# Kernel optimization log

Hardware: AMD Instinct MI355X
Metric: run time of the kernel (lower is better)

## Reference

```python
import jax, jax.numpy as jnp
import numpy as np

N = 100000   # nodes
E = 1600000  # edges (before self-loops)
G = 128      # graphs in batch
IN = 128     # in_channels
H = 64       # GCN hidden dim
OUT = 7      # out_channels
N_STACK = 9  # 64->64 GCN layers after the first


def setup_inputs() -> dict:
    key = jax.random.key(0)
    ks = jax.random.split(key, 10)
    s = 0.1
    x = jax.random.normal(ks[0], (N, IN), dtype=jnp.float32)
    edge_index = jax.random.randint(ks[1], (2, E), 0, N, dtype=jnp.int32)
    batch = jnp.sort(jax.random.randint(ks[2], (N,), 0, G, dtype=jnp.int32))
    W0 = jax.random.normal(ks[3], (IN, H), dtype=jnp.float32) * s
    b0 = jnp.zeros((H,), dtype=jnp.float32)
    Ws = jax.random.normal(ks[4], (N_STACK, H, H), dtype=jnp.float32) * s
    bs = jnp.zeros((N_STACK, H), dtype=jnp.float32)
    Wlin = jax.random.normal(ks[5], (H, OUT), dtype=jnp.float32) * s
    blin = jnp.zeros((OUT,), dtype=jnp.float32)
    return {"x": x, "edge_index": edge_index, "batch": batch,
            "W0": W0, "b0": b0, "Ws": Ws, "bs": bs,
            "Wlin": Wlin, "blin": blin}


def reference(x, edge_index, batch, W0, b0, Ws, bs, Wlin, blin):
    # GCNConv with add_self_loops=True, normalize=True (PyG defaults):
    # out = D^{-1/2} (A + I) D^{-1/2} (X W) + b
    loop = jnp.arange(N, dtype=edge_index.dtype)
    src = jnp.concatenate([edge_index[0], loop])   # [E+N]
    dst = jnp.concatenate([edge_index[1], loop])   # [E+N]
    ones = jnp.ones_like(dst, dtype=x.dtype)
    deg = jax.ops.segment_sum(ones, dst, num_segments=N)       # in-degree incl. self-loop
    dinv = jnp.where(deg > 0, jax.lax.rsqrt(deg), 0.0)
    norm = dinv[src] * dinv[dst]                                # [E+N]

    def gcn(h, W, b):
        m = h @ W                                               # [N,H] linear first
        agg = jax.ops.segment_sum(norm[:, None] * m[src], dst, num_segments=N)
        return agg + b

    h = jax.nn.relu(gcn(x, W0, b0))
    # nn.Dropout / EvalDropout are identity in the deterministic reference

    def step(h, wb):
        W, b = wb
        return jax.nn.relu(gcn(h, W, b)), None

    h, _ = jax.lax.scan(step, h, (Ws, bs))                      # 9 stacked GCN layers

    # global_mean_pool over graph ids
    counts = jax.ops.segment_sum(jnp.ones((N,), dtype=h.dtype), batch, num_segments=G)
    pooled = jax.ops.segment_sum(h, batch, num_segments=G) / jnp.clip(counts, 1.0)[:, None]
    return pooled @ Wlin + blin                                 # [G, OUT]
```

## Files before the change

kernel.cpp:

```cpp
#include <hip/hip_runtime.h>
#include <hip/hip_fp16.h>

#define NNODES 100000
#define NEDGES 1600000
#define NGRAPH 128
#define CIN 128
#define CH 64
#define COUT 7
#define NSTACK 9

#define NB 391
#define CHUNK 2048
#define NC 782

typedef __attribute__((ext_vector_type(8))) short bf16x8;
typedef __attribute__((ext_vector_type(4))) float f32x4;

__device__ __forceinline__ unsigned short f2bf(float f) {
    unsigned u = __float_as_uint(f);
    return (unsigned short)((u + 0x7FFFu + ((u >> 16) & 1u)) >> 16);
}

__global__ __launch_bounds__(256) void hist_gemm_kernel(const int* __restrict__ dst,
                                                        int* __restrict__ hist, int E,
                                                        const float* __restrict__ h,
                                                        const float* __restrict__ W,
                                                        __half* __restrict__ m, int N,
                                                        int histBlocks) {
    __shared__ alignas(16) char smem[32768 + 2048];
    if (blockIdx.x < (unsigned)histBlocks) {
        int* lh = (int*)smem;
        for (int i = threadIdx.x; i < NB; i += 256) lh[i] = 0;
        __syncthreads();
        int e0 = blockIdx.x * CHUNK;
        int e1 = min(e0 + CHUNK, E);
        for (int e = e0 + threadIdx.x; e < e1; e += 256)
            atomicAdd(&lh[dst[e] >> 8], 1);
        __syncthreads();
        for (int i = threadIdx.x; i < NB; i += 256) hist[i * NC + (int)blockIdx.x] = lh[i];
        return;
    }
    int gb = blockIdx.x - histBlocks;
    unsigned short* wf_hi = (unsigned short*)smem;
    unsigned short* wf_lo = wf_hi + 16 * 64 * 8;
    int t = threadIdx.x;

    {
        int c = t >> 4;
        int kstep = c >> 2, ncol = c & 3;
        int l0 = (t & 15) * 4;
        for (int dl = 0; dl < 4; ++dl) {
            int l = l0 + dl;
            int kbase = kstep * 32 + (l >> 4) * 8;
            int n = ncol * 16 + (l & 15);
            for (int i = 0; i < 8; ++i) {
                float wv = W[(size_t)(kbase + i) * 64 + n];
                unsigned short hb = f2bf(wv);
                float hf = __uint_as_float(((unsigned)hb) << 16);
                wf_hi[((size_t)c * 64 + l) * 8 + i] = hb;
                wf_lo[((size_t)c * 64 + l) * 8 + i] = f2bf(wv - hf);
            }
        }
    }
    __syncthreads();

    int wave = t >> 6, lane = t & 63;
    long row0 = (long)gb * 64 + wave * 16;
    if (row0 >= N) return;

    long arow = row0 + (lane & 15);
    const float4* xr = (const float4*)(h + (size_t)arow * 128);
    int kg = lane >> 4;

    f32x4 zero = {0.0f, 0.0f, 0.0f, 0.0f};
    f32x4 acc[4];
    acc[0] = zero; acc[1] = zero; acc[2] = zero; acc[3] = zero;

#pragma unroll
    for (int s = 0; s < 4; ++s) {
        float4 p = xr[s * 8 + kg * 2];
        float4 q = xr[s * 8 + kg * 2 + 1];
        float xv[8] = {p.x, p.y, p.z, p.w, q.x, q.y, q.z, q.w};
        bf16x8 a_hi, a_lo;
#pragma unroll
        for (int i = 0; i < 8; ++i) {
            unsigned short hb = f2bf(xv[i]);
            a_hi[i] = (short)hb;
            a_lo[i] = (short)f2bf(xv[i] - __uint_as_float(((unsigned)hb) << 16));
        }
#pragma unroll
        for (int nc = 0; nc < 4; ++nc) {
            int c = s * 4 + nc;
            bf16x8 b_hi = *(const bf16x8*)(wf_hi + ((size_t)c * 64 + lane) * 8);
            bf16x8 b_lo = *(const bf16x8*)(wf_lo + ((size_t)c * 64 + lane) * 8);
            acc[nc] = __builtin_amdgcn_mfma_f32_16x16x32_bf16(a_hi, b_hi, acc[nc], 0, 0, 0);
            acc[nc] = __builtin_amdgcn_mfma_f32_16x16x32_bf16(a_hi, b_lo, acc[nc], 0, 0, 0);
            acc[nc] = __builtin_amdgcn_mfma_f32_16x16x32_bf16(a_lo, b_hi, acc[nc], 0, 0, 0);
        }
    }

    int drow = (lane >> 4) * 4;
    int dcol = lane & 15;
#pragma unroll
    for (int nc = 0; nc < 4; ++nc)
#pragma unroll
        for (int r = 0; r < 4; ++r)
            m[(size_t)(row0 + drow + r) * 64 + nc * 16 + dcol] = __float2half(acc[nc][r]);
}

__global__ __launch_bounds__(256) void scan_chunks_kernel(int* __restrict__ hist,
                                                          int* __restrict__ btot) {
    int b = blockIdx.x;
    int t = threadIdx.x;
    int* row = hist + b * NC;
    int v[4];
    int base = 4 * t;
#pragma unroll
    for (int u = 0; u < 4; ++u) v[u] = (base + u < NC) ? row[base + u] : 0;
    int tsum = v[0] + v[1] + v[2] + v[3];
    __shared__ int s[256];
    s[t] = tsum;
    __syncthreads();
    for (int d = 1; d < 256; d <<= 1) {
        int x = (t >= d) ? s[t - d] : 0;
        __syncthreads();
        s[t] += x;
        __syncthreads();
    }
    int run = s[t] - tsum;
    if (t == 255) btot[b] = s[255];
#pragma unroll
    for (int u = 0; u < 4; ++u) {
        if (base + u < NC) row[base + u] = run;
        run += v[u];
    }
}

__global__ void scan_buckets_kernel(const int* __restrict__ tot, int* __restrict__ out) {
    __shared__ int s[512];
    int t = threadIdx.x;
    int v = (t < NB) ? tot[t] : 0;
    s[t] = v;
    __syncthreads();
    for (int d = 1; d < 512; d <<= 1) {
        int x = (t >= d) ? s[t - d] : 0;
        __syncthreads();
        s[t] += x;
        __syncthreads();
    }
    if (t < NB) out[t] = s[t] - v;
    if (t == NB - 1) out[NB] = s[t];
}

__global__ __launch_bounds__(256) void scatter_kernel(const int* __restrict__ src,
                                                      const int* __restrict__ dst,
                                                      const int* __restrict__ hist,
                                                      const int* __restrict__ bbase,
                                                      int* __restrict__ src_b,
                                                      int* __restrict__ dst_b, int E) {
    __shared__ int offs[NB];
    for (int b = threadIdx.x; b < NB; b += 256)
        offs[b] = hist[b * NC + (int)blockIdx.x] + bbase[b];
    __syncthreads();
    int e0 = blockIdx.x * CHUNK;
    int e1 = min(e0 + CHUNK, E);
    for (int e = e0 + threadIdx.x; e < e1; e += 256) {
        int d = dst[e], s = src[e];
        int pos = atomicAdd(&offs[d >> 8], 1);
        src_b[pos] = s;
        dst_b[pos] = d;
    }
}

__global__ __launch_bounds__(256) void bucket_prep_kernel(const int* __restrict__ dst_b,
                                                          const int* __restrict__ bbase,
                                                          const int* __restrict__ btot,
                                                          int* __restrict__ rowptr,
                                                          int* __restrict__ pbt,
                                                          float* __restrict__ dinv,
                                                          const int* __restrict__ batch,
                                                          int* __restrict__ gcnt, int N) {
    if ((int)blockIdx.x == NB) {
        int g = threadIdx.x;
        if (g >= NGRAPH) return;
        auto lb = [&](int v) {
            int lo = 0, hi = N;
            while (lo < hi) {
                int mid = (lo + hi) >> 1;
                if (batch[mid] < v) lo = mid + 1; else hi = mid;
            }
            return lo;
        };
        gcnt[g] = lb(g + 1) - lb(g);
        return;
    }
    __shared__ int c256[256];
    __shared__ int s[256];
    int t = threadIdx.x;
    c256[t] = 0;
    __syncthreads();
    int lo = bbase[blockIdx.x], n = btot[blockIdx.x];
    for (int e = lo + t; e < lo + n; e += 256) atomicAdd(&c256[dst_b[e] & 255], 1);
    __syncthreads();
    int cnt = c256[t];
    int pcnt = (cnt + 7) & ~7;
    s[t] = pcnt;
    __syncthreads();
    for (int d = 1; d < 256; d <<= 1) {
        int x = (t >= d) ? s[t - d] : 0;
        __syncthreads();
        s[t] += x;
        __syncthreads();
    }
    int node = blockIdx.x * 256 + t;
    if (node < N) {
        rowptr[node] = s[t] - pcnt;
        dinv[node] = 1.0f / sqrtf((float)(cnt + 1));
    }
    if (t == 255) pbt[blockIdx.x] = s[255];
}

__global__ void rowptr_fix_kernel(int* __restrict__ rowptr, const int* __restrict__ pbbase,
                                  int N) {
    int i = blockIdx.x * 256 + threadIdx.x;
    if (i < N) rowptr[i] += pbbase[i >> 8];
    if (i == 0) rowptr[N] = pbbase[NB];
}

__global__ __launch_bounds__(256) void bucket_fill_kernel(const int* __restrict__ src_b,
                                                          const int* __restrict__ dst_b,
                                                          const int* __restrict__ bbase,
                                                          const int* __restrict__ btot,
                                                          const int* __restrict__ rowptr,
                                                          int* __restrict__ col, int N) {
    __shared__ int f256[256];
    __shared__ int rp[256];
    int t = threadIdx.x;
    f256[t] = 0;
    int node = blockIdx.x * 256 + t;
    rp[t] = (node < N) ? rowptr[node] : 0;
    __syncthreads();
    int lo = bbase[blockIdx.x], n = btot[blockIdx.x];
    for (int e = lo + t; e < lo + n; e += 256) {
        int d = dst_b[e], sv = src_b[e];
        int li = d & 255;
        int slot = atomicAdd(&f256[li], 1);
        col[rp[li] + slot] = sv;
    }
    __syncthreads();
    if (node < N) {
        int c = f256[t];
        int pc = (c + 7) & ~7;
        int base = rp[t];
        for (int p = c; p < pc; ++p) col[base + p] = N;
    }
}

__global__ __launch_bounds__(256) void scale_m_kernel(__half* __restrict__ m,
                                                      __half* __restrict__ other,
                                                      const float* __restrict__ dinv, int N) {
    if (blockIdx.x == 0 && threadIdx.x < 64) {
        m[(size_t)N * 64 + threadIdx.x] = __float2half(0.0f);
        other[(size_t)N * 64 + threadIdx.x] = __float2half(0.0f);
    }
    int tot = N * 32;
    __half2* m2 = (__half2*)m;
    for (int idx = blockIdx.x * 256 + threadIdx.x; idx < tot; idx += gridDim.x * 256) {
        float d = dinv[idx >> 5];
        float2 f = __half22float2(m2[idx]);
        f.x *= d;
        f.y *= d;
        m2[idx] = __float22half2_rn(f);
    }
}

__device__ __forceinline__ void pair_gather(const __half* __restrict__ h,
                                            const int* __restrict__ col,
                                            int r0, int mid, int r1, int lane,
                                            float& aA, float& aB) {
    int n = r1 - r0;
    int e = 0;
    for (; e + 16 <= n; e += 16) {
        int base = r0 + e;
        int c[16];
        float v[16];
#pragma unroll
        for (int u = 0; u < 16; ++u) c[u] = col[base + u];
#pragma unroll
        for (int u = 0; u < 16; ++u) v[u] = __half2float(h[(size_t)c[u] * 64 + lane]);
        float s0 = ((v[0] + v[1]) + (v[2] + v[3])) + ((v[4] + v[5]) + (v[6] + v[7]));
        float s1 = ((v[8] + v[9]) + (v[10] + v[11])) + ((v[12] + v[13]) + (v[14] + v[15]));
        bool b0 = (base < mid);
        bool b1 = (base + 8 < mid);
        aA += b0 ? s0 : 0.0f;
        aB += b0 ? 0.0f : s0;
        aA += b1 ? s1 : 0.0f;
        aB += b1 ? 0.0f : s1;
    }
    if (e + 8 <= n) {
        int base = r0 + e;
        int c[8];
        float v[8];
#pragma unroll
        for (int u = 0; u < 8; ++u) c[u] = col[base + u];
#pragma unroll
        for (int u = 0; u < 8; ++u) v[u] = __half2float(h[(size_t)c[u] * 64 + lane]);
        float s0 = ((v[0] + v[1]) + (v[2] + v[3])) + ((v[4] + v[5]) + (v[6] + v[7]));
        bool b0 = (base < mid);
        aA += b0 ? s0 : 0.0f;
        aB += b0 ? 0.0f : s0;
    }
}

__global__ __launch_bounds__(256) void agg0_kernel(const __half* __restrict__ m,
                                                   const int* __restrict__ rowptr,
                                                   const int* __restrict__ col,
                                                   const float* __restrict__ dinv,
                                                   const float* __restrict__ bias,
                                                   __half* __restrict__ hout, int N) {
    int wid = __builtin_amdgcn_readfirstlane((blockIdx.x * 256 + threadIdx.x) >> 6);
    int lane = threadIdx.x & 63;
    int nodeA = wid * 2;
    int nodeB = nodeA + 1;
    if (nodeA >= N) return;
    int r0 = rowptr[nodeA];
    int mid = rowptr[nodeB];
    int r1 = rowptr[nodeB + 1];
    float diA = dinv[nodeA], diB = dinv[nodeB];
    float aA = __half2float(m[(size_t)nodeA * 64 + lane]);
    float aB = __half2float(m[(size_t)nodeB * 64 + lane]);
    pair_gather(m, col, r0, mid, r1, lane, aA, aB);
    float bv = bias[lane];
    float hA = fmaxf(diA * aA + bv, 0.0f);
    float hB = fmaxf(diB * aB + bv, 0.0f);
    hout[(size_t)nodeA * 64 + lane] = __float2half(diA * hA);
    hout[(size_t)nodeB * 64 + lane] = __float2half(diB * hB);
}

__global__ __launch_bounds__(256) void fused_kernel(const __half* __restrict__ h,
                                                    const int* __restrict__ rowptr,
                                                    const int* __restrict__ col,
                                                    const float* __restrict__ dinv,
                                                    const float* __restrict__ W,
                                                    const float* __restrict__ bias,
                                                    __half* __restrict__ hout, int N,
                                                    int scaleOut) {
    __shared__ float Ws[64 * 64];
    {
        const float4* W4 = (const float4*)W;
        float4* Ws4 = (float4*)Ws;
        for (int i = threadIdx.x; i < 64 * 16; i += 256) Ws4[i] = W4[i];
    }

    int wid = __builtin_amdgcn_readfirstlane((blockIdx.x * 256 + threadIdx.x) >> 6);
    int lane = threadIdx.x & 63;
    int nodeA = wid * 2;
    int nodeB = nodeA + 1;
    bool act = (nodeA < N);
    float gA = 0.0f, gB = 0.0f;
    float diA = 0.0f, diB = 0.0f;

    if (act) {
        int r0 = rowptr[nodeA];
        int mid = rowptr[nodeB];
        int r1 = rowptr[nodeB + 1];
        diA = dinv[nodeA];
        diB = dinv[nodeB];
        float aA = __half2float(h[(size_t)nodeA * 64 + lane]);
        float aB = __half2float(h[(size_t)nodeB * 64 + lane]);
        pair_gather(h, col, r0, mid, r1, lane, aA, aB);
        gA = diA * aA;
        gB = diB * aB;
    }

    __syncthreads();

    if (act) {
        float bv = bias[lane];
        float accA = bv, accB = bv;
#pragma unroll
        for (int k = 0; k < 64; ++k) {
            float wv = Ws[k * 64 + lane];
            unsigned ga = __builtin_amdgcn_readlane(__float_as_uint(gA), k);
            unsigned gb = __builtin_amdgcn_readlane(__float_as_uint(gB), k);
            accA += __uint_as_float(ga) * wv;
            accB += __uint_as_float(gb) * wv;
        }
        accA = fmaxf(accA, 0.0f);
        accB = fmaxf(accB, 0.0f);
        if (scaleOut) { accA *= diA; accB *= diB; }
        hout[(size_t)nodeA * 64 + lane] = __float2half(accA);
        hout[(size_t)nodeB * 64 + lane] = __float2half(accB);
    }
}

__global__ __launch_bounds__(256) void pool_kernel(const __half* __restrict__ h,
                                                   const int* __restrict__ batch,
                                                   float* __restrict__ gpool, int N) {
    const int NPW = 32;
    int wid = (blockIdx.x * 256 + threadIdx.x) >> 6;
    int lane = threadIdx.x & 63;
    int i0 = wid * NPW;
    if (i0 >= N) return;
    int i1 = min(i0 + NPW, N);
    int curg = batch[i0];
    float acc = 0.0f;
    for (int i = i0; i < i1; ++i) {
        int g = batch[i];
        if (g != curg) {
            atomicAdd(&gpool[curg * 64 + lane], acc);
            acc = 0.0f;
            curg = g;
        }
        acc += __half2float(h[(size_t)i * 64 + lane]);
    }
    atomicAdd(&gpool[curg * 64 + lane], acc);
}

__global__ void final_kernel(const float* __restrict__ gpool, const int* __restrict__ gcnt,
                             const float* __restrict__ Wlin, const float* __restrict__ blin,
                             float* __restrict__ out) {
    int t = threadIdx.x;
    if (t >= NGRAPH * COUT) return;
    int g = t / COUT, o = t - g * COUT;
    float c = (float)gcnt[g];
    if (c < 1.0f) c = 1.0f;
    float s = 0.0f;
    for (int k = 0; k < 64; ++k) s += gpool[g * 64 + k] * Wlin[k * COUT + o];
    out[t] = s / c + blin[o];
}

extern "C" void kernel_launch(void* const* d_in, const int* in_sizes, int n_in,
                              void* d_out, int out_size, void* d_ws, size_t ws_size,
                              hipStream_t stream) {
    const float* x    = (const float*)d_in[0];
    const int*   ei   = (const int*)d_in[1];
    const int*   batch= (const int*)d_in[2];
    const float* W0   = (const float*)d_in[3];
    const float* b0   = (const float*)d_in[4];
    const float* Ws   = (const float*)d_in[5];
    const float* bs   = (const float*)d_in[6];
    const float* Wlin = (const float*)d_in[7];
    const float* blin = (const float*)d_in[8];
    float* out = (float*)d_out;

    const int N = NNODES, E = NEDGES;
    const int* srcp = ei;
    const int* dstp = ei + E;

    char* w = (char*)d_ws;
    float* gpool  = (float*)w; w += (size_t)NGRAPH * 64 * 4;
    size_t zero_bytes = (size_t)(w - (char*)d_ws);
    int*   gcnt   = (int*)w;   w += (size_t)NGRAPH * 4;
    float* dinv   = (float*)w; w += (size_t)N * 4;
    int*   rowptr = (int*)w;   w += (size_t)(N + 1) * 4;
    int*   hist   = (int*)w;   w += (size_t)NB * NC * 4;
    int*   btot   = (int*)w;   w += (size_t)NB * 4;
    int*   bbase  = (int*)w;   w += (size_t)(NB + 1) * 4;
    int*   pbt    = (int*)w;   w += (size_t)NB * 4;
    int*   pbbase = (int*)w;   w += (size_t)(NB + 1) * 4;
    int*   src_b  = (int*)w;   w += (size_t)E * 4;
    int*   dst_b  = (int*)w;   w += (size_t)E * 4;
    int*   col    = (int*)w;   w += ((size_t)E + 8 * N) * 4;
    __half* bufA  = (__half*)w; w += (size_t)(N + 1) * 64 * 2;
    __half* bufB  = (__half*)w; w += (size_t)(N + 1) * 64 * 2;

    hipMemsetAsync(d_ws, 0, zero_bytes, stream);

    int nblocks = (N + 255) / 256;
    int gemmblocks = (N + 63) / 64;

    hist_gemm_kernel<<<NC + gemmblocks, 256, 0, stream>>>(
        dstp, hist, E, x, W0, bufB, N, NC);
    scan_chunks_kernel<<<NB, 256, 0, stream>>>(hist, btot);
    scan_buckets_kernel<<<1, 512, 0, stream>>>(btot, bbase);
    scatter_kernel<<<NC, 256, 0, stream>>>(srcp, dstp, hist, bbase, src_b, dst_b, E);
    bucket_prep_kernel<<<NB + 1, 256, 0, stream>>>(dst_b, bbase, btot, rowptr, pbt, dinv,
                                                   batch, gcnt, N);
    scan_buckets_kernel<<<1, 512, 0, stream>>>(pbt, pbbase);
    rowptr_fix_kernel<<<nblocks, 256, 0, stream>>>(rowptr, pbbase, N);
    bucket_fill_kernel<<<NB, 256, 0, stream>>>(src_b, dst_b, bbase, btot, rowptr, col, N);
    scale_m_kernel<<<2048, 256, 0, stream>>>(bufB, bufA, dinv, N);

    int pairblocks = (N / 2 + 3) / 4;

    agg0_kernel<<<pairblocks, 256, 0, stream>>>(bufB, rowptr, col, dinv, b0, bufA, N);

    __half* hin = bufA;
    __half* hout = bufB;
    for (int l = 0; l < NSTACK; ++l) {
        int scaleOut = (l < NSTACK - 1) ? 1 : 0;
        fused_kernel<<<pairblocks, 256, 0, stream>>>(hin, rowptr, col, dinv,
                                                     Ws + (size_t)l * 64 * 64,
                                                     bs + (size_t)l * 64, hout, N,
                                                     scaleOut);
        __half* t = hin; hin = hout; hout = t;
    }

    int pwaves = (N + 31) / 32;
    int pblocks = (pwaves + 3) / 4;
    pool_kernel<<<pblocks, 256, 0, stream>>>(hin, batch, gpool, N);
    final_kernel<<<1, 896, 0, stream>>>(gpool, gcnt, Wlin, blin, out);
}
```

Measured before the change: 650.7 us.

## Use split-bf16 MFMA for per-layer 64x64 transform in fused GCN kernel

Replaces the scalar readlane/FMA dense transform in the fused aggregate+linear kernel with bf16 MFMA using a hi/lo split (three MFMAs) to keep near-fp32 accuracy. Weights are pre-packed once into MFMA fragment layout by a new kernel, which removes the per-block 16KB shared-memory weight load. Gathered rows are staged in a small LDS tile so each wave computes one 16-column slice for the block's 8 nodes. This adds conversion work, and half of each 16-row MFMA tile is padding. The active-node guard is dropped, so it relies on N being divisible by 8.

After: 626.5 us. 3.7% less time.

```diff
diff --git a/kernel.cpp b/kernel.cpp
--- a/kernel.cpp
+++ b/kernel.cpp
@@ -106,6 +106,25 @@
 #pragma unroll
         for (int r = 0; r < 4; ++r)
             m[(size_t)(row0 + drow + r) * 64 + nc * 16 + dcol] = __float2half(acc[nc][r]);
+}
+
+__global__ void pack_wfrags_kernel(const float* __restrict__ Ws,
+                                   unsigned short* __restrict__ wfh,
+                                   unsigned short* __restrict__ wfl) {
+    int b = blockIdx.x;
+    int l = b >> 3, c = b & 7;
+    int s = c >> 2, nc = c & 3;
+    for (int v = threadIdx.x; v < 512; v += 256) {
+        int L = v >> 3, i = v & 7;
+        int k = s * 32 + (L >> 4) * 8 + i;
+        int n = nc * 16 + (L & 15);
+        float w = Ws[(size_t)l * 4096 + k * 64 + n];
+        unsigned short hb = f2bf(w);
+        float hf = __uint_as_float(((unsigned)hb) << 16);
+        size_t idx = ((size_t)b * 64 + L) * 8 + i;
+        wfh[idx] = hb;
+        wfl[idx] = f2bf(w - hf);
+    }
 }
 
 __global__ __launch_bounds__(256) void scan_chunks_kernel(int* __restrict__ hist,
@@ -341,56 +360,70 @@
                                                     const int* __restrict__ rowptr,
                                                     const int* __restrict__ col,
                                                     const float* __restrict__ dinv,
-                                                    const float* __restrict__ W,
+                                                    const unsigned short* __restrict__ wfh,
+                                                    const unsigned short* __restrict__ wfl,
                                                     const float* __restrict__ bias,
                                                     __half* __restrict__ hout, int N,
                                                     int scaleOut) {
-    __shared__ float Ws[64 * 64];
-    {
-        const float4* W4 = (const float4*)W;
-        float4* Ws4 = (float4*)Ws;
-        for (int i = threadIdx.x; i < 64 * 16; i += 256) Ws4[i] = W4[i];
-    }
-
-    int wid = __builtin_amdgcn_readfirstlane((blockIdx.x * 256 + threadIdx.x) >> 6);
+    __shared__ float gLds[16][68];
+
+    int wave = __builtin_amdgcn_readfirstlane((int)(threadIdx.x >> 6));
     int lane = threadIdx.x & 63;
-    int nodeA = wid * 2;
+    int node0 = blockIdx.x * 8;
+    int nodeA = node0 + wave * 2;
     int nodeB = nodeA + 1;
-    bool act = (nodeA < N);
-    float gA = 0.0f, gB = 0.0f;
-    float diA = 0.0f, diB = 0.0f;
-
-    if (act) {
-        int r0 = rowptr[nodeA];
-        int mid = rowptr[nodeB];
-        int r1 = rowptr[nodeB + 1];
-        diA = dinv[nodeA];
-        diB = dinv[nodeB];
-        float aA = __half2float(h[(size_t)nodeA * 64 + lane]);
-        float aB = __half2float(h[(size_t)nodeB * 64 + lane]);
-        pair_gather(h, col, r0, mid, r1, lane, aA, aB);
-        gA = diA * aA;
-        gB = diB * aB;
-    }
-
-    __syncthreads();
-
-    if (act) {
-        float bv = bias[lane];
-        float accA = bv, accB = bv;
-#pragma unroll
-        for (int k = 0; k < 64; ++k) {
-            float wv = Ws[k * 64 + lane];
-            unsigned ga = __builtin_amdgcn_readlane(__float_as_uint(gA), k);
-            unsigned gb = __builtin_amdgcn_readlane(__float_as_uint(gB), k);
-            accA += __uint_as_float(ga) * wv;
-            accB += __uint_as_float(gb) * wv;
+
+    int r0 = rowptr[nodeA];
+    int mid = rowptr[nodeB];
+    int r1 = rowptr[nodeB + 1];
+    float diA = dinv[nodeA], diB = dinv[nodeB];
+    float aA = __half2float(h[(size_t)nodeA * 64 + lane]);
+    float aB = __half2float(h[(size_t)nodeB * 64 + lane]);
+    pair_gather(h, col, r0, mid, r1, lane, aA, aB);
+    gLds[wave * 2][lane] = diA * aA;
+    gLds[wave * 2 + 1][lane] = diB * aB;
+
+    __syncthreads();
+
+    int arow = lane & 15;
+    int kg = lane >> 4;
+    f32x4 acc = {0.0f, 0.0f, 0.0f, 0.0f};
+#pragma unroll
+    for (int s = 0; s < 2; ++s) {
+        const float* ap = &gLds[arow][s * 32 + kg * 8];
+        float xv[8];
+#pragma unroll
+        for (int i = 0; i < 8; ++i) xv[i] = ap[i];
+        union { bf16x8 v; unsigned u[4]; } ahi, alo;
+#pragma unroll
+        for (int p = 0; p < 4; ++p) {
+            unsigned u0 = __float_as_uint(xv[2 * p]);
+            unsigned u1 = __float_as_uint(xv[2 * p + 1]);
+            ahi.u[p] = __builtin_amdgcn_perm(u1, u0, 0x07060302);
+            float l0 = xv[2 * p] - __uint_as_float(u0 & 0xFFFF0000u);
+            float l1 = xv[2 * p + 1] - __uint_as_float(u1 & 0xFFFF0000u);
+            unsigned r;
+            asm("v_cvt_pk_bf16_f32 %0, %1, %2" : "=v"(r) : "v"(l0), "v"(l1));
+            alo.u[p] = r;
         }
-        accA = fmaxf(accA, 0.0f);
-        accB = fmaxf(accB, 0.0f);
-        if (scaleOut) { accA *= diA; accB *= diB; }
-        hout[(size_t)nodeA * 64 + lane] = __float2half(accA);
-        hout[(size_t)nodeB * 64 + lane] = __float2half(accB);
+        const bf16x8 b_hi = *(const bf16x8*)(wfh + ((size_t)(s * 4 + wave) * 64 + lane) * 8);
+        const bf16x8 b_lo = *(const bf16x8*)(wfl + ((size_t)(s * 4 + wave) * 64 + lane) * 8);
+        acc = __builtin_amdgcn_mfma_f32_16x16x32_bf16(ahi.v, b_hi, acc, 0, 0, 0);
+        acc = __builtin_amdgcn_mfma_f32_16x16x32_bf16(ahi.v, b_lo, acc, 0, 0, 0);
+        acc = __builtin_amdgcn_mfma_f32_16x16x32_bf16(alo.v, b_hi, acc, 0, 0, 0);
+    }
+
+    int dcol = wave * 16 + (lane & 15);
+    int rbase = (lane >> 4) * 4;
+    if (rbase < 8) {
+        float bv = bias[dcol];
+#pragma unroll
+        for (int r = 0; r < 4; ++r) {
+            int nd = node0 + rbase + r;
+            float v = fmaxf(acc[r] + bv, 0.0f);
+            if (scaleOut) v *= dinv[nd];
+            hout[(size_t)nd * 64 + dcol] = __float2half(v);
+        }
     }
 }
 
@@ -462,6 +495,8 @@
     int*   src_b  = (int*)w;   w += (size_t)E * 4;
     int*   dst_b  = (int*)w;   w += (size_t)E * 4;
     int*   col    = (int*)w;   w += ((size_t)E + 8 * N) * 4;
+    unsigned short* wfh = (unsigned short*)w; w += (size_t)NSTACK * 4096 * 2;
+    unsigned short* wfl = (unsigned short*)w; w += (size_t)NSTACK * 4096 * 2;
     __half* bufA  = (__half*)w; w += (size_t)(N + 1) * 64 * 2;
     __half* bufB  = (__half*)w; w += (size_t)(N + 1) * 64 * 2;
 
@@ -470,6 +505,7 @@
     int nblocks = (N + 255) / 256;
     int gemmblocks = (N + 63) / 64;
 
+    pack_wfrags_kernel<<<NSTACK * 8, 256, 0, stream>>>(Ws, wfh, wfl);
     hist_gemm_kernel<<<NC + gemmblocks, 256, 0, stream>>>(
         dstp, hist, E, x, W0, bufB, N, NC);
     scan_chunks_kernel<<<NB, 256, 0, stream>>>(hist, btot);
@@ -483,6 +519,7 @@
     scale_m_kernel<<<2048, 256, 0, stream>>>(bufB, bufA, dinv, N);
 
     int pairblocks = (N / 2 + 3) / 4;
+    int fusedblocks = N / 8;
 
     agg0_kernel<<<pairblocks, 256, 0, stream>>>(bufB, rowptr, col, dinv, b0, bufA, N);
 
@@ -490,10 +527,11 @@
     __half* hout = bufB;
     for (int l = 0; l < NSTACK; ++l) {
         int scaleOut = (l < NSTACK - 1) ? 1 : 0;
-        fused_kernel<<<pairblocks, 256, 0, stream>>>(hin, rowptr, col, dinv,
-                                                     Ws + (size_t)l * 64 * 64,
-                                                     bs + (size_t)l * 64, hout, N,
-                                                     scaleOut);
+        fused_kernel<<<fusedblocks, 256, 0, stream>>>(hin, rowptr, col, dinv,
+                                                      wfh + (size_t)l * 4096,
+                                                      wfl + (size_t)l * 4096,
+                                                      bs + (size_t)l * 64, hout, N,
+                                                      scaleOut);
         __half* t = hin; hin = hout; hout = t;
     }
 
```
